# Performance work log

Measured on AMD Instinct MI355X. Metric: run time of the kernel, lower is better.

The kernel has to match this reference:

```python
import jax, jax.numpy as jnp
import numpy as np

B, NIN, NOUT, K = 1024, 126, 126, 3
H1, H2 = 256, 256

def _linear_params(key, out_f, in_f):
    # torch nn.Linear default init: U(-1/sqrt(in_f), 1/sqrt(in_f))
    bound = 1.0 / np.sqrt(in_f)
    kw, kb = jax.random.split(key)
    W = jax.random.uniform(kw, (out_f, in_f), minval=-bound, maxval=bound, dtype=jnp.float32)
    b = jax.random.uniform(kb, (out_f,), minval=-bound, maxval=bound, dtype=jnp.float32)
    return W, b

def setup_inputs() -> dict:
    key = jax.random.key(0)
    k0, k1, k2, kx, ki, ko = jax.random.split(key, 6)
    W0, b0 = _linear_params(k0, H1, NIN)
    W1, b1 = _linear_params(k1, H2, H1)
    W2, b2 = _linear_params(k2, NOUT, H2)
    x = jax.random.normal(kx, (B, NIN), dtype=jnp.float32)
    batch_in_index = jax.random.randint(ki, (B, NIN, K), 0, NIN + 1)   # NIN is zero-pad row
    batch_out_index = jax.random.randint(ko, (B, NOUT, K), 0, NOUT + 1)  # NOUT is zero-pad row
    return dict(x=x, W0=W0, b0=b0, W1=W1, b1=b1, W2=W2, b2=b2,
                batch_in_index=batch_in_index, batch_out_index=batch_out_index)

def reference(x, W0, b0, W1, b1, W2, b2, batch_in_index, batch_out_index):
    # --- layer 0: BatchIndexedLinear with batch_in_index ---
    # padded weight: (nin+1, h1), last row zeros
    pw0 = jnp.concatenate([W0.T, jnp.zeros((1, W0.shape[0]), W0.dtype)], axis=0)
    bw0 = pw0[batch_in_index].sum(-2)                 # (B, nin, h1)
    h = jnp.einsum('bi,bio->bo', x, bw0) + b0          # (B, h1)
    h = jax.nn.elu(h)
    # --- layer 1: plain linear ---
    h = jax.nn.elu(h @ W1.T + b1)                      # (B, h2)
    # --- layer 2: BatchIndexedLinear with batch_out_index ---
    pw2 = jnp.concatenate([W2, jnp.zeros((1, W2.shape[1]), W2.dtype)], axis=0)  # (nout+1, h2)
    g = pw2[batch_out_index].sum(-2)                   # (B, nout, h2)
    pb2 = jnp.concatenate([b2, jnp.zeros((1,), b2.dtype)])
    bb = pb2[batch_out_index].sum(-1)                  # (B, nout)
    return jnp.einsum('bh,boh->bo', h, g) + bb         # (B, nout)
```

## Files before the change

### kernel.cpp

```cpp
#include <hip/hip_runtime.h>

#define B_    1024
#define NIN_  126
#define NOUT_ 126
#define K_    3
#define H1_   256
#define H2_   256
#define RPB   4
#define TPB   512

__device__ __forceinline__ float elu1(float v) { return v > 0.0f ? v : expm1f(v); }

template<int CTRL>
__device__ __forceinline__ float dpp_add(float v) {
    int s = __builtin_amdgcn_update_dpp(0, __float_as_int(v), CTRL, 0xF, 0xF, true);
    return v + __int_as_float(s);
}
__device__ __forceinline__ float qsum8(float v) {
    v = dpp_add<0xB1>(v);
    v = dpp_add<0x4E>(v);
    int s = __builtin_amdgcn_ds_swizzle(__float_as_int(v), 0x101F);
    return v + __int_as_float(s);
}

__device__ __forceinline__ void barrier_lds() {
    asm volatile("s_waitcnt lgkmcnt(0)\n\ts_barrier" ::: "memory");
}

__global__ __launch_bounds__(TPB) void bim_fused(
    const float* __restrict__ x,  const float* __restrict__ W0,
    const float* __restrict__ b0, const float* __restrict__ W1,
    const float* __restrict__ b1, const float* __restrict__ W2,
    const float* __restrict__ b2, const int*  __restrict__ iidx,
    const int*  __restrict__ oidx, float* __restrict__ out)
{
    __shared__ float xe [RPB][128];
    __shared__ float h1s[RPB][H1_];
    __shared__ float h2s[RPB][H2_];
    __shared__ float ts [RPB][128];

    const int tid  = threadIdx.x;
    const int row0 = blockIdx.x * RPB;
    const int q    = tid & 7;
    const int g    = tid >> 3;

    int aj0, aj1, aj2, ar0, ar1, ar2; float ax0, ax1, ax2;
    {
        const int n0 = tid;
        ar0 = n0 / (NIN_ * K_); const int m0 = n0 - ar0 * (NIN_ * K_);
        aj0 = iidx[(row0 + ar0) * (NIN_ * K_) + m0];
        ax0 = x[(row0 + ar0) * NIN_ + m0 / K_];
        const int n1 = tid + TPB;
        ar1 = n1 / (NIN_ * K_); const int m1 = n1 - ar1 * (NIN_ * K_);
        aj1 = iidx[(row0 + ar1) * (NIN_ * K_) + m1];
        ax1 = x[(row0 + ar1) * NIN_ + m1 / K_];
        const int n2 = tid + 2 * TPB;
        const int n2c = n2 < RPB * NIN_ * K_ ? n2 : 0;
        ar2 = n2c / (NIN_ * K_); const int m2 = n2c - ar2 * (NIN_ * K_);
        aj2 = iidx[(row0 + ar2) * (NIN_ * K_) + m2];
        ax2 = x[(row0 + ar2) * NIN_ + m2 / K_];
        if (n2 >= RPB * NIN_ * K_) aj2 = NIN_;
    }

    const float* wb = W0 + (g * 4) * NIN_;
    float2 wA[4][4], wB[4][4];
    #pragma unroll
    for (int jj = 0; jj < 4; ++jj) {
        const int j  = q * 4 + jj * 32;
        const int j2 = (j + 2 > NIN_ - 2) ? (NIN_ - 2) : (j + 2);
        #pragma unroll
        for (int oo = 0; oo < 4; ++oo) {
            wA[jj][oo] = *reinterpret_cast<const float2*>(wb + oo * NIN_ + j);
            wB[jj][oo] = *reinterpret_cast<const float2*>(wb + oo * NIN_ + j2);
        }
    }

    int ej0, ej1, ej2;
    {
        const int t = tid < RPB * NOUT_ ? tid : 0;
        const int r = t / NOUT_, o = t - r * NOUT_;
        const int base = (row0 + r) * (NOUT_ * K_) + o * K_;
        ej0 = oidx[base]; ej1 = oidx[base + 1]; ej2 = oidx[base + 2];
    }
    const float4 b0v = *reinterpret_cast<const float4*>(b0 + g * 4);
    const float4 b1v = *reinterpret_cast<const float4*>(b1 + g * 4);
    const int    gD  = (g < 63) ? g : 0;
    const float2 b2v = *reinterpret_cast<const float2*>(b2 + gD * 2);

    (&xe[0][0])[tid] = 0.0f;
    barrier_lds();
    if (aj0 < NIN_) atomicAdd(&xe[ar0][aj0], ax0);
    if (aj1 < NIN_) atomicAdd(&xe[ar1][aj1], ax1);
    if (aj2 < NIN_) atomicAdd(&xe[ar2][aj2], ax2);

    const float* wcp = W1 + (g * 4) * H1_ + q * 4;
    float4 wc1[4][4];
    #pragma unroll
    for (int jj = 0; jj < 4; ++jj)
        #pragma unroll
        for (int oo = 0; oo < 4; ++oo)
            wc1[jj][oo] = *reinterpret_cast<const float4*>(wcp + oo * H1_ + jj * 32);
    barrier_lds();

    float4 wc2[4][4];
    {
        float acc[4][4] = {};
        #pragma unroll
        for (int jj = 0; jj < 2; ++jj) {
            const int j = q * 4 + jj * 32;
            float4 a[RPB];
            #pragma unroll
            for (int r = 0; r < RPB; ++r)
                a[r] = *reinterpret_cast<const float4*>(&xe[r][j]);
            #pragma unroll
            for (int oo = 0; oo < 4; ++oo)
                #pragma unroll
                for (int r = 0; r < RPB; ++r) {
                    acc[oo][r] = fmaf(wA[jj][oo].x, a[r].x, acc[oo][r]);
                    acc[oo][r] = fmaf(wA[jj][oo].y, a[r].y, acc[oo][r]);
                    acc[oo][r] = fmaf(wB[jj][oo].x, a[r].z, acc[oo][r]);
                    acc[oo][r] = fmaf(wB[jj][oo].y, a[r].w, acc[oo][r]);
                }
        }
        #pragma unroll
        for (int jj = 0; jj < 4; ++jj)
            #pragma unroll
            for (int oo = 0; oo < 4; ++oo)
                wc2[jj][oo] = *reinterpret_cast<const float4*>(wcp + oo * H1_ + (jj + 4) * 32);
        #pragma unroll
        for (int jj = 2; jj < 4; ++jj) {
            const int j = q * 4 + jj * 32;
            float4 a[RPB];
            #pragma unroll
            for (int r = 0; r < RPB; ++r)
                a[r] = *reinterpret_cast<const float4*>(&xe[r][j]);
            #pragma unroll
            for (int oo = 0; oo < 4; ++oo)
                #pragma unroll
                for (int r = 0; r < RPB; ++r) {
                    acc[oo][r] = fmaf(wA[jj][oo].x, a[r].x, acc[oo][r]);
                    acc[oo][r] = fmaf(wA[jj][oo].y, a[r].y, acc[oo][r]);
                    acc[oo][r] = fmaf(wB[jj][oo].x, a[r].z, acc[oo][r]);
                    acc[oo][r] = fmaf(wB[jj][oo].y, a[r].w, acc[oo][r]);
                }
        }
        #pragma unroll
        for (int oo = 0; oo < 4; ++oo)
            #pragma unroll
            for (int r = 0; r < RPB; ++r) acc[oo][r] = qsum8(acc[oo][r]);
        float v0 = acc[0][0], v1 = acc[0][1];
        #pragma unroll
        for (int i = 1; i < 8; ++i) {
            v0 = (q == i) ? acc[(2 * i) >> 2][(2 * i) & 3]         : v0;
            v1 = (q == i) ? acc[(2 * i + 1) >> 2][(2 * i + 1) & 3] : v1;
        }
        const int oo = q >> 1, r0 = (q & 1) * 2;
        const float bias = (oo == 0) ? b0v.x : (oo == 1) ? b0v.y : (oo == 2) ? b0v.z : b0v.w;
        const int o = g * 4 + oo;
        h1s[r0][o]     = elu1(v0 + bias);
        h1s[r0 + 1][o] = elu1(v1 + bias);
    }
    barrier_lds();

    const float* wdp = W2 + (gD * 2) * H2_ + q * 4;
    float4 wd[8][2];
    {
        float acc[4][4] = {};
        #pragma unroll
        for (int jj = 0; jj < 6; ++jj) {
            const float4* wrow = (jj < 4) ? wc1[jj] : wc2[jj - 4];
            const int j = q * 4 + jj * 32;
            float4 a[RPB];
            #pragma unroll
            for (int r = 0; r < RPB; ++r)
                a[r] = *reinterpret_cast<const float4*>(&h1s[r][j]);
            #pragma unroll
            for (int oo = 0; oo < 4; ++oo)
                #pragma unroll
                for (int r = 0; r < RPB; ++r) {
                    acc[oo][r] = fmaf(wrow[oo].x, a[r].x, acc[oo][r]);
                    acc[oo][r] = fmaf(wrow[oo].y, a[r].y, acc[oo][r]);
                    acc[oo][r] = fmaf(wrow[oo].z, a[r].z, acc[oo][r]);
                    acc[oo][r] = fmaf(wrow[oo].w, a[r].w, acc[oo][r]);
                }
        }
        #pragma unroll
        for (int jj = 0; jj < 8; ++jj)
            #pragma unroll
            for (int oo = 0; oo < 2; ++oo)
                wd[jj][oo] = *reinterpret_cast<const float4*>(wdp + oo * H2_ + jj * 32);
        #pragma unroll
        for (int jj = 6; jj < 8; ++jj) {
            const float4* wrow = wc2[jj - 4];
            const int j = q * 4 + jj * 32;
            float4 a[RPB];
            #pragma unroll
            for (int r = 0; r < RPB; ++r)
                a[r] = *reinterpret_cast<const float4*>(&h1s[r][j]);
            #pragma unroll
            for (int oo = 0; oo < 4; ++oo)
                #pragma unroll
                for (int r = 0; r < RPB; ++r) {
                    acc[oo][r] = fmaf(wrow[oo].x, a[r].x, acc[oo][r]);
                    acc[oo][r] = fmaf(wrow[oo].y, a[r].y, acc[oo][r]);
                    acc[oo][r] = fmaf(wrow[oo].z, a[r].z, acc[oo][r]);
                    acc[oo][r] = fmaf(wrow[oo].w, a[r].w, acc[oo][r]);
                }
        }
        #pragma unroll
        for (int oo = 0; oo < 4; ++oo)
            #pragma unroll
            for (int r = 0; r < RPB; ++r) acc[oo][r] = qsum8(acc[oo][r]);
        float v0 = acc[0][0], v1 = acc[0][1];
        #pragma unroll
        for (int i = 1; i < 8; ++i) {
            v0 = (q == i) ? acc[(2 * i) >> 2][(2 * i) & 3]         : v0;
            v1 = (q == i) ? acc[(2 * i + 1) >> 2][(2 * i + 1) & 3] : v1;
        }
        const int oo = q >> 1, r0 = (q & 1) * 2;
        const float bias = (oo == 0) ? b1v.x : (oo == 1) ? b1v.y : (oo == 2) ? b1v.z : b1v.w;
        const int o = g * 4 + oo;
        h2s[r0][o]     = elu1(v0 + bias);
        h2s[r0 + 1][o] = elu1(v1 + bias);
    }
    barrier_lds();

    {
        float acc[2][4] = {};
        #pragma unroll
        for (int jj = 0; jj < 8; ++jj) {
            const int j = q * 4 + jj * 32;
            float4 a[RPB];
            #pragma unroll
            for (int r = 0; r < RPB; ++r)
                a[r] = *reinterpret_cast<const float4*>(&h2s[r][j]);
            #pragma unroll
            for (int oo = 0; oo < 2; ++oo)
                #pragma unroll
                for (int r = 0; r < RPB; ++r) {
                    acc[oo][r] = fmaf(wd[jj][oo].x, a[r].x, acc[oo][r]);
                    acc[oo][r] = fmaf(wd[jj][oo].y, a[r].y, acc[oo][r]);
                    acc[oo][r] = fmaf(wd[jj][oo].z, a[r].z, acc[oo][r]);
                    acc[oo][r] = fmaf(wd[jj][oo].w, a[r].w, acc[oo][r]);
                }
        }
        #pragma unroll
        for (int oo = 0; oo < 2; ++oo)
            #pragma unroll
            for (int r = 0; r < RPB; ++r) acc[oo][r] = qsum8(acc[oo][r]);
        float v = acc[0][0];
        #pragma unroll
        for (int i = 1; i < 8; ++i) v = (q == i) ? acc[i >> 2][i & 3] : v;
        const int oo = q >> 2, rr = q & 3;
        if (g < 63) ts[rr][g * 2 + oo] = v + (oo ? b2v.y : b2v.x);
        else        ts[rr][126 + oo]   = 0.0f;
    }
    barrier_lds();

    if (tid < RPB * NOUT_) {
        const int r = tid / NOUT_, o = tid - r * NOUT_;
        out[(row0 + r) * NOUT_ + o] = ts[r][ej0] + ts[r][ej1] + ts[r][ej2];
    }
}

extern "C" void kernel_launch(void* const* d_in, const int* in_sizes, int n_in,
                              void* d_out, int out_size, void* d_ws, size_t ws_size,
                              hipStream_t stream) {
    const float* x   = (const float*)d_in[0];
    const float* W0  = (const float*)d_in[1];
    const float* b0  = (const float*)d_in[2];
    const float* W1  = (const float*)d_in[3];
    const float* b1  = (const float*)d_in[4];
    const float* W2  = (const float*)d_in[5];
    const float* b2  = (const float*)d_in[6];
    const int*  iidx = (const int*)d_in[7];
    const int*  oidx = (const int*)d_in[8];
    float* out = (float*)d_out;

    bim_fused<<<B_ / RPB, TPB, 0, stream>>>(x, W0, b0, W1, b1, W2, b2, iidx, oidx, out);
}
```

Before: 15.62 us.

## Convert weights to bf16 in a prepass kernel and load packed bf16 weights

Adds a small conversion kernel that rounds W0, W1 and W2 to bf16 into the workspace, with W0 padded to 128 columns. The fused kernel then loads packed bf16 pairs and expands them to fp32 before the FMAs. This halves per-block weight traffic and register footprint, since each of the 256 blocks rereads all weights. In exchange it adds a second launch and extra unpack instructions, and weight rounding lowers accuracy.

After: 19.82 us. +26.9%, slower.

```diff
diff --git a/kernel.cpp b/kernel.cpp
--- a/kernel.cpp
+++ b/kernel.cpp
@@ -9,6 +9,11 @@
 #define RPB   4
 #define TPB   512
 
+#define W0BF_OFF 0
+#define W1BF_OFF 32768
+#define W2BF_OFF 98304
+#define WBF_TOTAL 130560
+
 __device__ __forceinline__ float elu1(float v) { return v > 0.0f ? v : expm1f(v); }
 
 template<int CTRL>
@@ -27,12 +32,37 @@
     asm volatile("s_waitcnt lgkmcnt(0)\n\ts_barrier" ::: "memory");
 }
 
+__device__ __forceinline__ unsigned short f2bf(float f) {
+    unsigned u = __float_as_uint(f);
+    u = (u + 0x7FFFu + ((u >> 16) & 1u)) >> 16;
+    return (unsigned short)u;
+}
+__device__ __forceinline__ float2 bf2f(unsigned u) {
+    return make_float2(__uint_as_float(u << 16), __uint_as_float(u & 0xFFFF0000u));
+}
+
+__global__ __launch_bounds__(256) void wconv(
+    const float* __restrict__ W0, const float* __restrict__ W1,
+    const float* __restrict__ W2, unsigned short* __restrict__ wsb)
+{
+    const int t = blockIdx.x * 256 + threadIdx.x;
+    if (t < 32768) {
+        const int o = t >> 7, j = t & 127;
+        wsb[W0BF_OFF + t] = (j < NIN_) ? f2bf(W0[o * NIN_ + j]) : (unsigned short)0;
+    } else if (t < 98304) {
+        const int e = t - 32768;
+        wsb[W1BF_OFF + e] = f2bf(W1[e]);
+    } else if (t < WBF_TOTAL) {
+        const int e = t - 98304;
+        wsb[W2BF_OFF + e] = f2bf(W2[e]);
+    }
+}
+
 __global__ __launch_bounds__(TPB) void bim_fused(
-    const float* __restrict__ x,  const float* __restrict__ W0,
-    const float* __restrict__ b0, const float* __restrict__ W1,
-    const float* __restrict__ b1, const float* __restrict__ W2,
-    const float* __restrict__ b2, const int*  __restrict__ iidx,
-    const int*  __restrict__ oidx, float* __restrict__ out)
+    const float* __restrict__ x,  const unsigned short* __restrict__ wsb,
+    const float* __restrict__ b0, const float* __restrict__ b1,
+    const float* __restrict__ b2, const int* __restrict__ iidx,
+    const int* __restrict__ oidx, float* __restrict__ out)
 {
     __shared__ float xe [RPB][128];
     __shared__ float h1s[RPB][H1_];
@@ -62,18 +92,13 @@
         if (n2 >= RPB * NIN_ * K_) aj2 = NIN_;
     }
 
-    const float* wb = W0 + (g * 4) * NIN_;
-    float2 wA[4][4], wB[4][4];
+    const unsigned short* w0b = wsb + W0BF_OFF + (g * 4) * 128 + q * 4;
+    uint2 wb[4][4];
     #pragma unroll
-    for (int jj = 0; jj < 4; ++jj) {
-        const int j  = q * 4 + jj * 32;
-        const int j2 = (j + 2 > NIN_ - 2) ? (NIN_ - 2) : (j + 2);
-        #pragma unroll
-        for (int oo = 0; oo < 4; ++oo) {
-            wA[jj][oo] = *reinterpret_cast<const float2*>(wb + oo * NIN_ + j);
-            wB[jj][oo] = *reinterpret_cast<const float2*>(wb + oo * NIN_ + j2);
-        }
-    }
+    for (int jj = 0; jj < 4; ++jj)
+        #pragma unroll
+        for (int oo = 0; oo < 4; ++oo)
+            wb[jj][oo] = *reinterpret_cast<const uint2*>(w0b + oo * 128 + jj * 32);
 
     int ej0, ej1, ej2;
     {
@@ -93,16 +118,16 @@
     if (aj1 < NIN_) atomicAdd(&xe[ar1][aj1], ax1);
     if (aj2 < NIN_) atomicAdd(&xe[ar2][aj2], ax2);
 
-    const float* wcp = W1 + (g * 4) * H1_ + q * 4;
-    float4 wc1[4][4];
+    const unsigned short* wcp = wsb + W1BF_OFF + (g * 4) * H1_ + q * 4;
+    uint2 wc1[4][4];
     #pragma unroll
     for (int jj = 0; jj < 4; ++jj)
         #pragma unroll
         for (int oo = 0; oo < 4; ++oo)
-            wc1[jj][oo] = *reinterpret_cast<const float4*>(wcp + oo * H1_ + jj * 32);
-    barrier_lds();
-
-    float4 wc2[4][4];
+            wc1[jj][oo] = *reinterpret_cast<const uint2*>(wcp + oo * H1_ + jj * 32);
+    barrier_lds();
+
+    uint2 wc2[4][4];
     {
         float acc[4][4] = {};
         #pragma unroll
@@ -113,20 +138,23 @@
             for (int r = 0; r < RPB; ++r)
                 a[r] = *reinterpret_cast<const float4*>(&xe[r][j]);
             #pragma unroll
+            for (int oo = 0; oo < 4; ++oo) {
+                const float2 p0 = bf2f(wb[jj][oo].x);
+                const float2 p1 = bf2f(wb[jj][oo].y);
+                #pragma unroll
+                for (int r = 0; r < RPB; ++r) {
+                    acc[oo][r] = fmaf(p0.x, a[r].x, acc[oo][r]);
+                    acc[oo][r] = fmaf(p0.y, a[r].y, acc[oo][r]);
+                    acc[oo][r] = fmaf(p1.x, a[r].z, acc[oo][r]);
+                    acc[oo][r] = fmaf(p1.y, a[r].w, acc[oo][r]);
+                }
+            }
+        }
+        #pragma unroll
+        for (int jj = 0; jj < 4; ++jj)
+            #pragma unroll
             for (int oo = 0; oo < 4; ++oo)
-                #pragma unroll
-                for (int r = 0; r < RPB; ++r) {
-                    acc[oo][r] = fmaf(wA[jj][oo].x, a[r].x, acc[oo][r]);
-                    acc[oo][r] = fmaf(wA[jj][oo].y, a[r].y, acc[oo][r]);
-                    acc[oo][r] = fmaf(wB[jj][oo].x, a[r].z, acc[oo][r]);
-                    acc[oo][r] = fmaf(wB[jj][oo].y, a[r].w, acc[oo][r]);
-                }
-        }
-        #pragma unroll
-        for (int jj = 0; jj < 4; ++jj)
-            #pragma unroll
-            for (int oo = 0; oo < 4; ++oo)
-                wc2[jj][oo] = *reinterpret_cast<const float4*>(wcp + oo * H1_ + (jj + 4) * 32);
+                wc2[jj][oo] = *reinterpret_cast<const uint2*>(wcp + oo * H1_ + (jj + 4) * 32);
         #pragma unroll
         for (int jj = 2; jj < 4; ++jj) {
             const int j = q * 4 + jj * 32;
@@ -135,14 +163,17 @@
             for (int r = 0; r < RPB; ++r)
                 a[r] = *reinterpret_cast<const float4*>(&xe[r][j]);
             #pragma unroll
-            for (int oo = 0; oo < 4; ++oo)
-                #pragma unroll
-                for (int r = 0; r < RPB; ++r) {
-                    acc[oo][r] = fmaf(wA[jj][oo].x, a[r].x, acc[oo][r]);
-                    acc[oo][r] = fmaf(wA[jj][oo].y, a[r].y, acc[oo][r]);
-                    acc[oo][r] = fmaf(wB[jj][oo].x, a[r].z, acc[oo][r]);
-                    acc[oo][r] = fmaf(wB[jj][oo].y, a[r].w, acc[oo][r]);
-                }
+            for (int oo = 0; oo < 4; ++oo) {
+                const float2 p0 = bf2f(wb[jj][oo].x);
+                const float2 p1 = bf2f(wb[jj][oo].y);
+                #pragma unroll
+                for (int r = 0; r < RPB; ++r) {
+                    acc[oo][r] = fmaf(p0.x, a[r].x, acc[oo][r]);
+                    acc[oo][r] = fmaf(p0.y, a[r].y, acc[oo][r]);
+                    acc[oo][r] = fmaf(p1.x, a[r].z, acc[oo][r]);
+                    acc[oo][r] = fmaf(p1.y, a[r].w, acc[oo][r]);
+                }
+            }
         }
         #pragma unroll
         for (int oo = 0; oo < 4; ++oo)
@@ -162,50 +193,56 @@
     }
     barrier_lds();
 
-    const float* wdp = W2 + (gD * 2) * H2_ + q * 4;
-    float4 wd[8][2];
+    const unsigned short* wdp = wsb + W2BF_OFF + (gD * 2) * H2_ + q * 4;
+    uint2 wd[8][2];
     {
         float acc[4][4] = {};
         #pragma unroll
         for (int jj = 0; jj < 6; ++jj) {
-            const float4* wrow = (jj < 4) ? wc1[jj] : wc2[jj - 4];
+            const uint2* wrow = (jj < 4) ? wc1[jj] : wc2[jj - 4];
             const int j = q * 4 + jj * 32;
             float4 a[RPB];
             #pragma unroll
             for (int r = 0; r < RPB; ++r)
                 a[r] = *reinterpret_cast<const float4*>(&h1s[r][j]);
             #pragma unroll
-            for (int oo = 0; oo < 4; ++oo)
-                #pragma unroll
-                for (int r = 0; r < RPB; ++r) {
-                    acc[oo][r] = fmaf(wrow[oo].x, a[r].x, acc[oo][r]);
-                    acc[oo][r] = fmaf(wrow[oo].y, a[r].y, acc[oo][r]);
-                    acc[oo][r] = fmaf(wrow[oo].z, a[r].z, acc[oo][r]);
-                    acc[oo][r] = fmaf(wrow[oo].w, a[r].w, acc[oo][r]);
-                }
+            for (int oo = 0; oo < 4; ++oo) {
+                const float2 p0 = bf2f(wrow[oo].x);
+                const float2 p1 = bf2f(wrow[oo].y);
+                #pragma unroll
+                for (int r = 0; r < RPB; ++r) {
+                    acc[oo][r] = fmaf(p0.x, a[r].x, acc[oo][r]);
+                    acc[oo][r] = fmaf(p0.y, a[r].y, acc[oo][r]);
+                    acc[oo][r] = fmaf(p1.x, a[r].z, acc[oo][r]);
+                    acc[oo][r] = fmaf(p1.y, a[r].w, acc[oo][r]);
+                }
+            }
         }
         #pragma unroll
         for (int jj = 0; jj < 8; ++jj)
             #pragma unroll
             for (int oo = 0; oo < 2; ++oo)
-                wd[jj][oo] = *reinterpret_cast<const float4*>(wdp + oo * H2_ + jj * 32);
+                wd[jj][oo] = *reinterpret_cast<const uint2*>(wdp + oo * H2_ + jj * 32);
         #pragma unroll
         for (int jj = 6; jj < 8; ++jj) {
-            const float4* wrow = wc2[jj - 4];
+            const uint2* wrow = wc2[jj - 4];
             const int j = q * 4 + jj * 32;
             float4 a[RPB];
             #pragma unroll
             for (int r = 0; r < RPB; ++r)
                 a[r] = *reinterpret_cast<const float4*>(&h1s[r][j]);
             #pragma unroll
-            for (int oo = 0; oo < 4; ++oo)
-                #pragma unroll
-                for (int r = 0; r < RPB; ++r) {
-                    acc[oo][r] = fmaf(wrow[oo].x, a[r].x, acc[oo][r]);
-                    acc[oo][r] = fmaf(wrow[oo].y, a[r].y, acc[oo][r]);
-                    acc[oo][r] = fmaf(wrow[oo].z, a[r].z, acc[oo][r]);
-                    acc[oo][r] = fmaf(wrow[oo].w, a[r].w, acc[oo][r]);
-                }
+            for (int oo = 0; oo < 4; ++oo) {
+                const float2 p0 = bf2f(wrow[oo].x);
+                const float2 p1 = bf2f(wrow[oo].y);
+                #pragma unroll
+                for (int r = 0; r < RPB; ++r) {
+                    acc[oo][r] = fmaf(p0.x, a[r].x, acc[oo][r]);
+                    acc[oo][r] = fmaf(p0.y, a[r].y, acc[oo][r]);
+                    acc[oo][r] = fmaf(p1.x, a[r].z, acc[oo][r]);
+                    acc[oo][r] = fmaf(p1.y, a[r].w, acc[oo][r]);
+                }
+            }
         }
         #pragma unroll
         for (int oo = 0; oo < 4; ++oo)
@@ -235,14 +272,17 @@
             for (int r = 0; r < RPB; ++r)
                 a[r] = *reinterpret_cast<const float4*>(&h2s[r][j]);
             #pragma unroll
-            for (int oo = 0; oo < 2; ++oo)
-                #pragma unroll
-                for (int r = 0; r < RPB; ++r) {
-                    acc[oo][r] = fmaf(wd[jj][oo].x, a[r].x, acc[oo][r]);
-                    acc[oo][r] = fmaf(wd[jj][oo].y, a[r].y, acc[oo][r]);
-                    acc[oo][r] = fmaf(wd[jj][oo].z, a[r].z, acc[oo][r]);
-                    acc[oo][r] = fmaf(wd[jj][oo].w, a[r].w, acc[oo][r]);
-                }
+            for (int oo = 0; oo < 2; ++oo) {
+                const float2 p0 = bf2f(wd[jj][oo].x);
+                const float2 p1 = bf2f(wd[jj][oo].y);
+                #pragma unroll
+                for (int r = 0; r < RPB; ++r) {
+                    acc[oo][r] = fmaf(p0.x, a[r].x, acc[oo][r]);
+                    acc[oo][r] = fmaf(p0.y, a[r].y, acc[oo][r]);
+                    acc[oo][r] = fmaf(p1.x, a[r].z, acc[oo][r]);
+                    acc[oo][r] = fmaf(p1.y, a[r].w, acc[oo][r]);
+                }
+            }
         }
         #pragma unroll
         for (int oo = 0; oo < 2; ++oo)
@@ -276,6 +316,8 @@
     const int*  iidx = (const int*)d_in[7];
     const int*  oidx = (const int*)d_in[8];
     float* out = (float*)d_out;
-
-    bim_fused<<<B_ / RPB, TPB, 0, stream>>>(x, W0, b0, W1, b1, W2, b2, iidx, oidx, out);
-}
+    unsigned short* wsb = (unsigned short*)d_ws;
+
+    wconv<<<512, 256, 0, stream>>>(W0, W1, W2, wsb);
+    bim_fused<<<B_ / RPB, TPB, 0, stream>>>(x, wsb, b0, b1, b2, iidx, oidx, out);
+}
```
